# Kernel tuning notes

Hardware: AMD Instinct MI355X
Metric: run time of the kernel (lower is better)

## Reference

```python
import jax, jax.numpy as jnp
import numpy as np

EPS = 1e-8

def setup_inputs() -> dict:
    key = jax.random.key(0)
    k0, k1, k2, k3, k4 = jax.random.split(key, 5)
    B, N, K, Q, L, F = 8, 5, 5, 4, 128, 768
    support_emb = jax.random.normal(k0, (B, N, K, L, F), dtype=jnp.float32)
    query_emb = jax.random.normal(k1, (B, N * Q, L, F), dtype=jnp.float32)
    B_mask = jax.random.randint(k2, (B, N, K, L), 0, 2, dtype=jnp.int32)
    I_mask = jax.random.randint(k3, (B, N, K, L), 0, 2, dtype=jnp.int32)
    trigger_label = jax.random.randint(k4, (B, N * Q, L), 0, 2 * N + 1, dtype=jnp.int32)
    return {"support_emb": support_emb, "query_emb": query_emb, "B_mask": B_mask,
            "I_mask": I_mask, "trigger_label": trigger_label, "N": N, "K": K, "Q": Q}

def _proto(support_emb, Bm, Im, N):
    # support_emb: (B,N,K,L,F); Bm/Im: (B,N,K,L) float
    sum_B = jnp.einsum('bnklf,bnkl->bnf', support_emb, Bm)
    cnt_B = Bm.sum((2, 3))[..., None] + EPS
    pB = sum_B / cnt_B                                   # (B,N,F)
    sum_I = jnp.einsum('bnklf,bnkl->bnf', support_emb, Im)
    cnt_I = Im.sum((2, 3))[..., None] + EPS
    pI = sum_I / cnt_I                                   # (B,N,F)
    Om = 1.0 - Bm - Im                                   # (B,N,K,L)
    sum_O = jnp.einsum('bnklf,bnkl->bf', support_emb, Om)
    cnt_O = Om.sum((1, 2, 3))[:, None] + EPS
    pO = sum_O / cnt_O                                   # (B,F)
    Bsz, F = pO.shape
    # interleave: tags [O, B_0, I_0, B_1, I_1, ...]
    pBI = jnp.stack([pB, pI], axis=2).reshape(Bsz, 2 * N, F)
    return jnp.concatenate([pO[:, None, :], pBI], axis=1)  # (B, 2N+1, F)

def reference(support_emb, query_emb, B_mask, I_mask, trigger_label, N, K, Q):
    dt = support_emb.dtype
    Bm = B_mask.astype(dt)
    Im = I_mask.astype(dt)
    prototype = _proto(support_emb, Bm, Im, N)             # (B, 2N+1, F)
    # similarity: broadcast dot product -> batched GEMM
    logits = jnp.einsum('bqlf,btf->bqlt', query_emb, prototype)  # (B, NQ, L, 2N+1)
    T = logits.shape[-1]
    flat = logits.reshape(-1, T)
    pred = jnp.argmax(flat, axis=1)
    lab = trigger_label.reshape(-1)
    logp = jax.nn.log_softmax(flat, axis=-1)
    loss = -jnp.take_along_axis(logp, lab[:, None], axis=1).mean()
    return (loss, logits, pred)
```

## Files before the change

kernel.cpp:

```cpp
#include <hip/hip_runtime.h>
#include <cstdint>
#include <cstddef>

#define EPS 1e-8f

#define Bsz 8
#define Nn  5
#define Kk  5
#define Ll  128
#define Ff  768
#define Tt  11
#define KL  640
#define ROWS_PER_B 2560
#define NROWS 20480
#define F4  192
#define BN  40

#define S1_ROWS 16
#define S1_CH   (KL / S1_ROWS)
#define S1_NBLK (BN * S1_CH)
#define PART_STRIDE (3 * Ff)
#define PART_STRIDE4 (PART_STRIDE / 4)

typedef float v2f __attribute__((ext_vector_type(2)));

__global__ __launch_bounds__(192) void stage1(
    const float* __restrict__ sup,
    const int*   __restrict__ Bm,
    const int*   __restrict__ Im,
    float* __restrict__ part,
    float* __restrict__ pcnt)
{
    int blk = blockIdx.x;
    int bn  = blk / S1_CH;
    int ch  = blk - bn * S1_CH;
    int tid = threadIdx.x;

    const float4* sp = (const float4*)(sup + ((size_t)bn * KL + ch * S1_ROWS) * Ff) + tid;
    const int*    bp = Bm + bn * KL + ch * S1_ROWS;
    const int*    ip = Im + bn * KL + ch * S1_ROWS;

    float4 v[S1_ROWS];
    #pragma unroll
    for (int p = 0; p < S1_ROWS; ++p) v[p] = sp[p * F4];

    int mb[S1_ROWS], mi[S1_ROWS];
    #pragma unroll
    for (int p = 0; p < S1_ROWS; ++p) { mb[p] = bp[p]; mi[p] = ip[p]; }

    v2f tB0 = {0.f,0.f}, tB1 = tB0, tI0 = tB0, tI1 = tB0, tA0 = tB0, tA1 = tB0;
    int cB = 0, cI = 0;

    #pragma unroll
    for (int p = 0; p < S1_ROWS; ++p) {
        v2f lo = {v[p].x, v[p].y};
        v2f hi = {v[p].z, v[p].w};
        tA0 += lo; tA1 += hi;
        if (mb[p]) { tB0 += lo; tB1 += hi; ++cB; }
        if (mi[p]) { tI0 += lo; tI1 += hi; ++cI; }
    }

    float4* o = (float4*)(part + (size_t)blk * PART_STRIDE);
    float4 rB = {tB0.x, tB0.y, tB1.x, tB1.y};
    float4 rI = {tI0.x, tI0.y, tI1.x, tI1.y};
    float4 rA = {tA0.x, tA0.y, tA1.x, tA1.y};
    o[tid]          = rB;
    o[F4 + tid]     = rI;
    o[2 * F4 + tid] = rA;

    if (tid == 0) {
        pcnt[2 * (size_t)blk]     = (float)cB;
        pcnt[2 * (size_t)blk + 1] = (float)cI;
    }
}

__global__ __launch_bounds__(256) void stage2(
    const float* __restrict__ part,
    float* __restrict__ bnsum,
    float* __restrict__ loss_out)
{
    int gid = blockIdx.x * 256 + threadIdx.x;
    if (gid == 0) loss_out[0] = 0.0f;

    int bn  = gid / (3 * F4);
    int r   = gid - bn * (3 * F4);
    int set = r / F4;
    int f4  = r - set * F4;

    const float4* src = (const float4*)(part + (size_t)bn * S1_CH * PART_STRIDE + set * Ff) + f4;
    float4 s = {0, 0, 0, 0};
    #pragma unroll
    for (int c8 = 0; c8 < S1_CH / 8; ++c8) {
        float4 v[8];
        #pragma unroll
        for (int j = 0; j < 8; ++j) v[j] = src[(size_t)(c8 * 8 + j) * PART_STRIDE4];
        #pragma unroll
        for (int j = 0; j < 8; ++j) {
            s.x += v[j].x; s.y += v[j].y; s.z += v[j].z; s.w += v[j].w;
        }
    }
    ((float4*)bnsum)[((size_t)bn * 3 + set) * F4 + f4] = s;
}

#define S3_ROWS 32
#define S3_NBLK (NROWS / S3_ROWS)
#define BLKS_PER_B (ROWS_PER_B / S3_ROWS)
#define SL  8
#define SW  24
#define LDS_T (SL * (SW + 1))

__global__ __launch_bounds__(256) void stage3(
    const float* __restrict__ query,
    const float* __restrict__ bnsum,
    const float* __restrict__ pcnt,
    const int*   __restrict__ label,
    float* __restrict__ out_logits,
    float* __restrict__ out_pred,
    float* __restrict__ loss_out)
{
    __shared__ float4 ldsP[Tt * LDS_T];
    __shared__ float  sCnt[2 * Nn];
    __shared__ float  sScale[Tt];

    int blk = blockIdx.x;
    int b   = blk / BLKS_PER_B;
    int tid = threadIdx.x;

    if (tid < 2 * Nn) sCnt[tid] = 0.0f;
    __syncthreads();
    for (int i = tid; i < 400; i += 256) {
        float v = pcnt[400 * b + i];
        int n   = i / 80;
        int set = i & 1;
        atomicAdd(&sCnt[2 * n + set], v);
    }
    __syncthreads();
    if (tid < Tt) {
        if (tid == 0) {
            float cO = (float)(KL * Nn);
            #pragma unroll
            for (int k = 0; k < 2 * Nn; ++k) cO -= sCnt[k];
            sScale[0] = 1.0f / (cO + EPS);
        } else {
            sScale[tid] = 1.0f / (sCnt[tid - 1] + EPS);
        }
    }
    __syncthreads();

    const float4* bs = (const float4*)bnsum + (size_t)b * Nn * 3 * F4;
    for (int idx = tid; idx < Tt * F4; idx += 256) {
        int t  = idx / F4;
        int f4 = idx - t * F4;
        float4 val;
        if (t == 0) {
            float sx = 0, sy = 0, sz = 0, sw = 0;
            #pragma unroll
            for (int n = 0; n < Nn; ++n) {
                float4 A  = bs[(n * 3 + 2) * F4 + f4];
                float4 Bv = bs[(n * 3 + 0) * F4 + f4];
                float4 Iv = bs[(n * 3 + 1) * F4 + f4];
                sx += A.x - Bv.x - Iv.x; sy += A.y - Bv.y - Iv.y;
                sz += A.z - Bv.z - Iv.z; sw += A.w - Bv.w - Iv.w;
            }
            val.x = sx; val.y = sy; val.z = sz; val.w = sw;
        } else {
            int n   = (t - 1) >> 1;
            int set = (t - 1) & 1;
            val = bs[(n * 3 + set) * F4 + f4];
        }
        float sc = sScale[t];
        val.x *= sc; val.y *= sc; val.z *= sc; val.w *= sc;
        int s = f4 / SW, j = f4 - SW * s;
        ldsP[t * LDS_T + s * (SW + 1) + j] = val;
    }
    __syncthreads();

    int w    = tid >> 6;
    int lane = tid & 63;
    int p    = lane >> 3;
    int s    = lane & 7;

    size_t row = (size_t)blk * S3_ROWS + w * 8 + p;
    const float4* q = (const float4*)(query + row * Ff) + s * SW;

    float acc[Tt];
    #pragma unroll
    for (int t = 0; t < Tt; ++t) acc[t] = 0.0f;

    const float4* pb = &ldsP[s * (SW + 1)];
    #pragma unroll
    for (int h = 0; h < 2; ++h) {
        float4 qv[12];
        #pragma unroll
        for (int j = 0; j < 12; ++j) qv[j] = q[h * 12 + j];
        #pragma unroll
        for (int j = 0; j < 12; ++j) {
            float4 u = qv[j];
            int jj = h * 12 + j;
            #pragma unroll
            for (int t = 0; t < Tt; ++t) {
                float4 pv = pb[t * LDS_T + jj];
                float d = acc[t];
                d = fmaf(u.x, pv.x, d); d = fmaf(u.y, pv.y, d);
                d = fmaf(u.z, pv.z, d); d = fmaf(u.w, pv.w, d);
                acc[t] = d;
            }
        }
    }

    #pragma unroll
    for (int t = 0; t < Tt; ++t) {
        acc[t] += __shfl_xor(acc[t], 1, 64);
        acc[t] += __shfl_xor(acc[t], 2, 64);
        acc[t] += __shfl_xor(acc[t], 4, 64);
    }

    float wloss = 0.0f;
    if (s == 0) {
        float m = acc[0]; int bt = 0;
        #pragma unroll
        for (int t = 1; t < Tt; ++t) if (acc[t] > m) { m = acc[t]; bt = t; }
        float sum = 0.0f;
        #pragma unroll
        for (int t = 0; t < Tt; ++t) sum += __expf(acc[t] - m);
        int lab = label[row];
        float labv = acc[0];
        #pragma unroll
        for (int t = 1; t < Tt; ++t) labv = (lab == t) ? acc[t] : labv;
        #pragma unroll
        for (int t = 0; t < Tt; ++t) out_logits[row * Tt + t] = acc[t];
        out_pred[row] = (float)bt;
        wloss = (m + __logf(sum)) - labv;
    }
    #pragma unroll
    for (int off = 32; off > 0; off >>= 1) wloss += __shfl_xor(wloss, off, 64);
    if (lane == 0) atomicAdd(loss_out, wloss * (1.0f / (float)NROWS));
}

extern "C" void kernel_launch(void* const* d_in, const int* in_sizes, int n_in,
                              void* d_out, int out_size, void* d_ws, size_t ws_size,
                              hipStream_t stream) {
    const float* sup   = (const float*)d_in[0];
    const float* query = (const float*)d_in[1];
    const int*   Bm    = (const int*)d_in[2];
    const int*   Im    = (const int*)d_in[3];
    const int*   lab   = (const int*)d_in[4];

    float* w     = (float*)d_ws;
    float* part  = w;
    float* pcnt  = part + (size_t)S1_NBLK * PART_STRIDE;
    float* bnsum = pcnt + 2 * S1_NBLK;

    float* loss_out   = (float*)d_out;
    float* out_logits = (float*)d_out + 1;
    float* out_pred   = (float*)d_out + 1 + (size_t)NROWS * Tt;

    stage1<<<S1_NBLK, 192, 0, stream>>>(sup, Bm, Im, part, pcnt);
    stage2<<<90, 256, 0, stream>>>(part, bnsum, loss_out);
    stage3<<<S3_NBLK, 256, 0, stream>>>(query, bnsum, pcnt, lab,
                                        out_logits, out_pred, loss_out);
}
```

Before: 212.9 us.

## Double-buffer loads in stage1 and stage3, double rows per stage1 block

Stage1 now processes 32 rows per block instead of 16, halving the number of partial-sum blocks and the partial buffer that stage2 reduces, and it prefetches the next 8 rows into an alternate register buffer while accumulating the current ones. Stage2 and the stage3 count loading are adjusted to the new chunk count. Stage3 splits the query loads into 6-element chunks, prefetching the next chunk while computing, and batches the LDS prototype reads per chunk. The aim is more overlap of global-memory latency with compute and a lighter stage2 reduction, at the cost of fewer stage1 blocks and different register pressure.

```diff
diff --git a/kernel.cpp b/kernel.cpp
--- a/kernel.cpp
+++ b/kernel.cpp
@@ -16,7 +16,7 @@
 #define F4  192
 #define BN  40
 
-#define S1_ROWS 16
+#define S1_ROWS 32
 #define S1_CH   (KL / S1_ROWS)
 #define S1_NBLK (BN * S1_CH)
 #define PART_STRIDE (3 * Ff)
@@ -40,24 +40,34 @@
     const int*    bp = Bm + bn * KL + ch * S1_ROWS;
     const int*    ip = Im + bn * KL + ch * S1_ROWS;
 
-    float4 v[S1_ROWS];
-    #pragma unroll
-    for (int p = 0; p < S1_ROWS; ++p) v[p] = sp[p * F4];
-
-    int mb[S1_ROWS], mi[S1_ROWS];
-    #pragma unroll
-    for (int p = 0; p < S1_ROWS; ++p) { mb[p] = bp[p]; mi[p] = ip[p]; }
+    float4 bufA[8], bufB[8];
+    #pragma unroll
+    for (int j = 0; j < 8; ++j) bufA[j] = sp[j * F4];
 
     v2f tB0 = {0.f,0.f}, tB1 = tB0, tI0 = tB0, tI1 = tB0, tA0 = tB0, tA1 = tB0;
     int cB = 0, cI = 0;
 
     #pragma unroll
-    for (int p = 0; p < S1_ROWS; ++p) {
-        v2f lo = {v[p].x, v[p].y};
-        v2f hi = {v[p].z, v[p].w};
-        tA0 += lo; tA1 += hi;
-        if (mb[p]) { tB0 += lo; tB1 += hi; ++cB; }
-        if (mi[p]) { tI0 += lo; tI1 += hi; ++cI; }
+    for (int h = 0; h < 4; ++h) {
+        if (h < 3) {
+            if ((h & 1) == 0) {
+                #pragma unroll
+                for (int j = 0; j < 8; ++j) bufB[j] = sp[((h + 1) * 8 + j) * F4];
+            } else {
+                #pragma unroll
+                for (int j = 0; j < 8; ++j) bufA[j] = sp[((h + 1) * 8 + j) * F4];
+            }
+        }
+        #pragma unroll
+        for (int j = 0; j < 8; ++j) {
+            int p = h * 8 + j;
+            float4 v = ((h & 1) == 0) ? bufA[j] : bufB[j];
+            v2f lo = {v.x, v.y};
+            v2f hi = {v.z, v.w};
+            tA0 += lo; tA1 += hi;
+            if (bp[p]) { tB0 += lo; tB1 += hi; ++cB; }
+            if (ip[p]) { tI0 += lo; tI1 += hi; ++cI; }
+        }
     }
 
     float4* o = (float4*)(part + (size_t)blk * PART_STRIDE);
@@ -90,12 +100,12 @@
     const float4* src = (const float4*)(part + (size_t)bn * S1_CH * PART_STRIDE + set * Ff) + f4;
     float4 s = {0, 0, 0, 0};
     #pragma unroll
-    for (int c8 = 0; c8 < S1_CH / 8; ++c8) {
-        float4 v[8];
-        #pragma unroll
-        for (int j = 0; j < 8; ++j) v[j] = src[(size_t)(c8 * 8 + j) * PART_STRIDE4];
-        #pragma unroll
-        for (int j = 0; j < 8; ++j) {
+    for (int c4 = 0; c4 < S1_CH / 4; ++c4) {
+        float4 v[4];
+        #pragma unroll
+        for (int j = 0; j < 4; ++j) v[j] = src[(size_t)(c4 * 4 + j) * PART_STRIDE4];
+        #pragma unroll
+        for (int j = 0; j < 4; ++j) {
             s.x += v[j].x; s.y += v[j].y; s.z += v[j].z; s.w += v[j].w;
         }
     }
@@ -128,10 +138,10 @@
 
     if (tid < 2 * Nn) sCnt[tid] = 0.0f;
     __syncthreads();
-    for (int i = tid; i < 400; i += 256) {
-        float v = pcnt[400 * b + i];
-        int n   = i / 80;
-        int set = i & 1;
+    if (tid < 200) {
+        float v = pcnt[200 * b + tid];
+        int n   = tid / 40;
+        int set = tid & 1;
         atomicAdd(&sCnt[2 * n + set], v);
     }
     __syncthreads();
@@ -188,21 +198,29 @@
     for (int t = 0; t < Tt; ++t) acc[t] = 0.0f;
 
     const float4* pb = &ldsP[s * (SW + 1)];
-    #pragma unroll
-    for (int h = 0; h < 2; ++h) {
-        float4 qv[12];
-        #pragma unroll
-        for (int j = 0; j < 12; ++j) qv[j] = q[h * 12 + j];
-        #pragma unroll
-        for (int j = 0; j < 12; ++j) {
-            float4 u = qv[j];
-            int jj = h * 12 + j;
+
+    float4 qv[2][6];
+    #pragma unroll
+    for (int j = 0; j < 6; ++j) qv[0][j] = q[j];
+
+    #pragma unroll
+    for (int h = 0; h < 4; ++h) {
+        if (h < 3) {
+            #pragma unroll
+            for (int j = 0; j < 6; ++j) qv[(h + 1) & 1][j] = q[(h + 1) * 6 + j];
+        }
+        #pragma unroll
+        for (int j2 = 0; j2 < 6; ++j2) {
+            int jj = h * 6 + j2;
+            float4 pv[Tt];
+            #pragma unroll
+            for (int t = 0; t < Tt; ++t) pv[t] = pb[t * LDS_T + jj];
+            float4 u = qv[h & 1][j2];
             #pragma unroll
             for (int t = 0; t < Tt; ++t) {
-                float4 pv = pb[t * LDS_T + jj];
                 float d = acc[t];
-                d = fmaf(u.x, pv.x, d); d = fmaf(u.y, pv.y, d);
-                d = fmaf(u.z, pv.z, d); d = fmaf(u.w, pv.w, d);
+                d = fmaf(u.x, pv[t].x, d); d = fmaf(u.y, pv[t].y, d);
+                d = fmaf(u.z, pv[t].z, d); d = fmaf(u.w, pv[t].w, d);
                 acc[t] = d;
             }
         }
```

New measurement: 212.1 us. No clear change (-0.4%).
